# Performance work log

Measured on AMD Instinct MI355X. Metric: run time of the kernel, lower is better.

The kernel has to match this reference:

```python
import jax, jax.numpy as jnp
import numpy as np


def setup_inputs() -> dict:
    key = jax.random.key(0)
    inputs = jax.random.normal(key, (4096, 8192), dtype=jnp.float32)
    return {"inputs": inputs, "k": 512}


def reference(inputs, k):
    # Original: kth_smallest = sort_ascending(inputs)[..., n-1-k]
    # i.e. the (k+1)-th largest value per row. Equivalent via top_k.
    # Keep only elements STRICTLY greater than that threshold.
    thresh = jax.lax.top_k(inputs, k + 1)[0][..., -1]  # [batch]
    mask = (inputs > thresh[:, None]).astype(inputs.dtype)
    return inputs * mask
```

## Files before the change

### kernel.cpp

```cpp
#include <hip/hip_runtime.h>
#include <stdint.h>


constexpr int COLS  = 8192;
constexpr int TPB   = 256;
constexpr int EPT   = COLS / TPB;
constexpr int VPT   = EPT / 4;
constexpr int NBIN0 = 2048;
constexpr int CAP   = 2048;

__device__ __forceinline__ uint32_t map_f32(uint32_t u) {
  return (u & 0x80000000u) ? ~u : (u | 0x80000000u);
}
__device__ __forceinline__ float unmap_f32(uint32_t m) {
  return __uint_as_float((m & 0x80000000u) ? (m ^ 0x80000000u) : ~m);
}

__global__ __launch_bounds__(TPB)
void ksparse_kernel(const float* __restrict__ in, const int* __restrict__ kptr,
                    float* __restrict__ out) {
  __shared__ __align__(16) uint32_t hist[2 * NBIN0];
  __shared__ uint32_t th[3 * 128];
  __shared__ uint32_t wtot[4];
  __shared__ uint32_t s_packed;
  __shared__ uint32_t s_cnt;
  __shared__ uint32_t s_sel[3];

  const int t    = threadIdx.x;
  const int wave = t >> 6;
  const int lane = t & 63;
  const size_t rowbase = (size_t)blockIdx.x * COLS;

  const float4* inp = (const float4*)(in + rowbase);
  float4 v[VPT];
#pragma unroll
  for (int i = 0; i < VPT; ++i) v[i] = inp[t + i * TPB];

  uint4* h4 = (uint4*)hist;
#pragma unroll
  for (int i = 0; i < 4; ++i) h4[t + i * TPB] = make_uint4(0u, 0u, 0u, 0u);
  th[t] = 0u;
  if (t < 128) th[256 + t] = 0u;
  if (t == 0) { s_packed = 0u; s_cnt = 0u; }
  uint32_t kk = (uint32_t)(*kptr) + 1u;
  __syncthreads();

  uint32_t m[EPT];
  uint32_t* h = &hist[(wave >> 1) * NBIN0];
#pragma unroll
  for (int i = 0; i < VPT; ++i) {
    m[4 * i + 0] = map_f32(__float_as_uint(v[i].x));
    m[4 * i + 1] = map_f32(__float_as_uint(v[i].y));
    m[4 * i + 2] = map_f32(__float_as_uint(v[i].z));
    m[4 * i + 3] = map_f32(__float_as_uint(v[i].w));
    atomicAdd(&h[m[4 * i + 0] >> 21], 1u);
    atomicAdd(&h[m[4 * i + 1] >> 21], 1u);
    atomicAdd(&h[m[4 * i + 2] >> 21], 1u);
    atomicAdd(&h[m[4 * i + 3] >> 21], 1u);
  }
  __syncthreads();

  {
    const uint4* hv = (const uint4*)hist;
    uint4 a0 = hv[2 * t], a1 = hv[2 * t + 1];
    uint4 b0 = hv[512 + 2 * t], b1 = hv[512 + 2 * t + 1];
    uint32_t c0 = a0.x + b0.x, c1 = a0.y + b0.y, c2 = a0.z + b0.z, c3 = a0.w + b0.w;
    uint32_t c4 = a1.x + b1.x, c5 = a1.y + b1.y, c6 = a1.z + b1.z, c7 = a1.w + b1.w;
    uint32_t sl[8];
    sl[7] = c7;         sl[6] = sl[7] + c6; sl[5] = sl[6] + c5; sl[4] = sl[5] + c4;
    sl[3] = sl[4] + c3; sl[2] = sl[3] + c2; sl[1] = sl[2] + c1; sl[0] = sl[1] + c0;
    const uint32_t total = sl[0];

    uint32_t s = total;
#pragma unroll
    for (int off = 1; off < 64; off <<= 1) {
      uint32_t tmp = __shfl_down(s, off, 64);
      s += (lane + off < 64) ? tmp : 0u;
    }
    if (lane == 0) wtot[wave] = s;
    __syncthreads();

    uint32_t hi = 0;
#pragma unroll
    for (int w = 1; w < 4; ++w)
      if (w > wave) hi += wtot[w];
    const uint32_t excl = hi + (s - total);

    int best = -1;
#pragma unroll
    for (int j = 7; j >= 0; --j)
      if (best < 0 && excl + sl[j] >= kk) best = j;
    if (best >= 0) {
      const uint32_t above = excl + ((best < 7) ? sl[best + 1] : 0u);
      atomicMax(&s_packed, ((uint32_t)(t * 8 + best) << 14) | above);
    }
  }
  __syncthreads();

  const uint32_t pk = s_packed;
  const uint32_t d0 = pk >> 14;
  kk -= (pk & 0x3FFFu);

  uint32_t* cand = &hist[NBIN0];
#pragma unroll
  for (int i = 0; i < EPT; ++i) {
    if ((m[i] >> 21) == d0) {
      uint32_t idx = atomicAdd(&s_cnt, 1u);
      if (idx < CAP) cand[idx] = m[i] & 0x1FFFFFu;
    }
  }
  __syncthreads();
  const uint32_t Cc = (s_cnt < (uint32_t)CAP) ? s_cnt : (uint32_t)CAP;

  uint32_t tpref = 0;
#pragma unroll 1
  for (int j = 0; j < 3; ++j) {
    const int dsh = 14 - 7 * j;
    uint32_t* thj = &th[j * 128];
    for (uint32_t idx = t; idx < Cc; idx += TPB) {
      const uint32_t c = cand[idx];
      const bool ok = (j == 0) || ((c >> (dsh + 7)) == tpref);
      if (ok) atomicAdd(&thj[(c >> dsh) & 127u], 1u);
    }
    __syncthreads();

    if (wave == 0) {
      uint32_t a = thj[lane], b = thj[64 + lane];
      uint32_t sb = b, sa = a;
#pragma unroll
      for (int off = 1; off < 64; off <<= 1) {
        uint32_t t1 = __shfl_down(sb, off, 64);
        uint32_t t2 = __shfl_down(sa, off, 64);
        const bool inr = (lane + off < 64);
        sb += inr ? t1 : 0u;
        sa += inr ? t2 : 0u;
      }
      const uint32_t tb = __shfl(sb, 0, 64);
      sa += tb;
      const unsigned long long mb = __ballot(sb >= kk);
      uint32_t d, ab;
      if (mb) {
        const int hb = 63 - __builtin_clzll(mb);
        const uint32_t nx = __shfl(sb, (hb + 1) & 63, 64);
        d = 64 + hb;
        ab = (hb == 63) ? 0u : nx;
      } else {
        const unsigned long long ma = __ballot(sa >= kk);
        const int ha = 63 - __builtin_clzll(ma);
        const uint32_t nx = __shfl(sa, (ha + 1) & 63, 64);
        d = (uint32_t)ha;
        ab = (ha == 63) ? tb : nx;
      }
      if (lane == 0) s_sel[j] = (d << 16) | ab;
    }
    __syncthreads();

    const uint32_t sel = s_sel[j];
    tpref = (tpref << 7) | (sel >> 16);
    kk -= (sel & 0xFFFFu);
  }

  const uint32_t T = (d0 << 21) | tpref;

  float4* op = (float4*)(out + rowbase);
#pragma unroll
  for (int i = 0; i < VPT; ++i) {
    float4 w;
    uint32_t mm;
    mm = m[4 * i + 0]; w.x = (mm > T) ? unmap_f32(mm) : 0.0f;
    mm = m[4 * i + 1]; w.y = (mm > T) ? unmap_f32(mm) : 0.0f;
    mm = m[4 * i + 2]; w.z = (mm > T) ? unmap_f32(mm) : 0.0f;
    mm = m[4 * i + 3]; w.w = (mm > T) ? unmap_f32(mm) : 0.0f;
    op[t + i * TPB] = w;
  }
}

extern "C" void kernel_launch(void* const* d_in, const int* in_sizes, int n_in,
                              void* d_out, int out_size, void* d_ws, size_t ws_size,
                              hipStream_t stream) {
  const float* in  = (const float*)d_in[0];
  const int*   k   = (const int*)d_in[1];
  float*       out = (float*)d_out;
  int rows = in_sizes[0] / COLS;
  if (rows < 1) rows = 1;
  ksparse_kernel<<<rows, TPB, 0, stream>>>(in, k, out);
}
```

Measured before the change: 234.8 us.

## Process four rows per block with register double-buffered prefetch of next row

Each block now handles four rows. The next row's loads are issued into a second register buffer while the current row's selection passes run, so global memory latency overlaps with the histogram work. Output writes become nontemporal stores, and launch bounds request 4 waves per SIMD. The costs are doubled register pressure for the prefetch buffer (64 extra VGPRs) and a grid cut from 4096 to 1024 blocks, which could reduce latency hiding across blocks.

```diff
diff --git a/kernel.cpp b/kernel.cpp
--- a/kernel.cpp
+++ b/kernel.cpp
@@ -9,6 +9,8 @@
 constexpr int NBIN0 = 2048;
 constexpr int CAP   = 2048;
 
+typedef float f32x4 __attribute__((ext_vector_type(4)));
+
 __device__ __forceinline__ uint32_t map_f32(uint32_t u) {
   return (u & 0x80000000u) ? ~u : (u | 0x80000000u);
 }
@@ -16,7 +18,8 @@
   return __uint_as_float((m & 0x80000000u) ? (m ^ 0x80000000u) : ~m);
 }
 
-__global__ __launch_bounds__(TPB)
+template <int RPB>
+__global__ __launch_bounds__(TPB, 4)
 void ksparse_kernel(const float* __restrict__ in, const int* __restrict__ kptr,
                     float* __restrict__ out) {
   __shared__ __align__(16) uint32_t hist[2 * NBIN0];
@@ -29,149 +32,163 @@
   const int t    = threadIdx.x;
   const int wave = t >> 6;
   const int lane = t & 63;
-  const size_t rowbase = (size_t)blockIdx.x * COLS;
-
-  const float4* inp = (const float4*)(in + rowbase);
-  float4 v[VPT];
-#pragma unroll
-  for (int i = 0; i < VPT; ++i) v[i] = inp[t + i * TPB];
-
-  uint4* h4 = (uint4*)hist;
-#pragma unroll
-  for (int i = 0; i < 4; ++i) h4[t + i * TPB] = make_uint4(0u, 0u, 0u, 0u);
-  th[t] = 0u;
-  if (t < 128) th[256 + t] = 0u;
-  if (t == 0) { s_packed = 0u; s_cnt = 0u; }
-  uint32_t kk = (uint32_t)(*kptr) + 1u;
-  __syncthreads();
-
+  const size_t row0 = (size_t)blockIdx.x * RPB;
+
+  const uint32_t kbase = (uint32_t)(*kptr) + 1u;
+
+  float4   v[2][VPT];
   uint32_t m[EPT];
-  uint32_t* h = &hist[(wave >> 1) * NBIN0];
-#pragma unroll
-  for (int i = 0; i < VPT; ++i) {
-    m[4 * i + 0] = map_f32(__float_as_uint(v[i].x));
-    m[4 * i + 1] = map_f32(__float_as_uint(v[i].y));
-    m[4 * i + 2] = map_f32(__float_as_uint(v[i].z));
-    m[4 * i + 3] = map_f32(__float_as_uint(v[i].w));
-    atomicAdd(&h[m[4 * i + 0] >> 21], 1u);
-    atomicAdd(&h[m[4 * i + 1] >> 21], 1u);
-    atomicAdd(&h[m[4 * i + 2] >> 21], 1u);
-    atomicAdd(&h[m[4 * i + 3] >> 21], 1u);
+
+  {
+    const float4* inp = (const float4*)(in + row0 * COLS);
+#pragma unroll
+    for (int i = 0; i < VPT; ++i) v[0][i] = inp[t + i * TPB];
   }
-  __syncthreads();
-
-  {
-    const uint4* hv = (const uint4*)hist;
-    uint4 a0 = hv[2 * t], a1 = hv[2 * t + 1];
-    uint4 b0 = hv[512 + 2 * t], b1 = hv[512 + 2 * t + 1];
-    uint32_t c0 = a0.x + b0.x, c1 = a0.y + b0.y, c2 = a0.z + b0.z, c3 = a0.w + b0.w;
-    uint32_t c4 = a1.x + b1.x, c5 = a1.y + b1.y, c6 = a1.z + b1.z, c7 = a1.w + b1.w;
-    uint32_t sl[8];
-    sl[7] = c7;         sl[6] = sl[7] + c6; sl[5] = sl[6] + c5; sl[4] = sl[5] + c4;
-    sl[3] = sl[4] + c3; sl[2] = sl[3] + c2; sl[1] = sl[2] + c1; sl[0] = sl[1] + c0;
-    const uint32_t total = sl[0];
-
-    uint32_t s = total;
-#pragma unroll
-    for (int off = 1; off < 64; off <<= 1) {
-      uint32_t tmp = __shfl_down(s, off, 64);
-      s += (lane + off < 64) ? tmp : 0u;
-    }
-    if (lane == 0) wtot[wave] = s;
-    __syncthreads();
-
-    uint32_t hi = 0;
-#pragma unroll
-    for (int w = 1; w < 4; ++w)
-      if (w > wave) hi += wtot[w];
-    const uint32_t excl = hi + (s - total);
-
-    int best = -1;
-#pragma unroll
-    for (int j = 7; j >= 0; --j)
-      if (best < 0 && excl + sl[j] >= kk) best = j;
-    if (best >= 0) {
-      const uint32_t above = excl + ((best < 7) ? sl[best + 1] : 0u);
-      atomicMax(&s_packed, ((uint32_t)(t * 8 + best) << 14) | above);
-    }
-  }
-  __syncthreads();
-
-  const uint32_t pk = s_packed;
-  const uint32_t d0 = pk >> 14;
-  kk -= (pk & 0x3FFFu);
-
-  uint32_t* cand = &hist[NBIN0];
-#pragma unroll
-  for (int i = 0; i < EPT; ++i) {
-    if ((m[i] >> 21) == d0) {
-      uint32_t idx = atomicAdd(&s_cnt, 1u);
-      if (idx < CAP) cand[idx] = m[i] & 0x1FFFFFu;
-    }
-  }
-  __syncthreads();
-  const uint32_t Cc = (s_cnt < (uint32_t)CAP) ? s_cnt : (uint32_t)CAP;
-
-  uint32_t tpref = 0;
+
+#pragma unroll
+  for (int r = 0; r < RPB; ++r) {
+    uint4* h4 = (uint4*)hist;
+#pragma unroll
+    for (int i = 0; i < 4; ++i) h4[t + i * TPB] = make_uint4(0u, 0u, 0u, 0u);
+    th[t] = 0u;
+    if (t < 128) th[256 + t] = 0u;
+    if (t == 0) { s_packed = 0u; s_cnt = 0u; }
+    uint32_t kk = kbase;
+    __syncthreads();
+
+    uint32_t* h = &hist[(wave >> 1) * NBIN0];
+#pragma unroll
+    for (int i = 0; i < VPT; ++i) {
+      m[4 * i + 0] = map_f32(__float_as_uint(v[r & 1][i].x));
+      m[4 * i + 1] = map_f32(__float_as_uint(v[r & 1][i].y));
+      m[4 * i + 2] = map_f32(__float_as_uint(v[r & 1][i].z));
+      m[4 * i + 3] = map_f32(__float_as_uint(v[r & 1][i].w));
+      atomicAdd(&h[m[4 * i + 0] >> 21], 1u);
+      atomicAdd(&h[m[4 * i + 1] >> 21], 1u);
+      atomicAdd(&h[m[4 * i + 2] >> 21], 1u);
+      atomicAdd(&h[m[4 * i + 3] >> 21], 1u);
+    }
+
+    if (r + 1 < RPB) {
+      const float4* inp = (const float4*)(in + (row0 + (size_t)(r + 1)) * COLS);
+#pragma unroll
+      for (int i = 0; i < VPT; ++i) v[(r + 1) & 1][i] = inp[t + i * TPB];
+    }
+    __syncthreads();
+
+    {
+      const uint4* hv = (const uint4*)hist;
+      uint4 a0 = hv[2 * t], a1 = hv[2 * t + 1];
+      uint4 b0 = hv[512 + 2 * t], b1 = hv[512 + 2 * t + 1];
+      uint32_t c0 = a0.x + b0.x, c1 = a0.y + b0.y, c2 = a0.z + b0.z, c3 = a0.w + b0.w;
+      uint32_t c4 = a1.x + b1.x, c5 = a1.y + b1.y, c6 = a1.z + b1.z, c7 = a1.w + b1.w;
+      uint32_t sl[8];
+      sl[7] = c7;         sl[6] = sl[7] + c6; sl[5] = sl[6] + c5; sl[4] = sl[5] + c4;
+      sl[3] = sl[4] + c3; sl[2] = sl[3] + c2; sl[1] = sl[2] + c1; sl[0] = sl[1] + c0;
+      const uint32_t total = sl[0];
+
+      uint32_t s = total;
+#pragma unroll
+      for (int off = 1; off < 64; off <<= 1) {
+        uint32_t tmp = __shfl_down(s, off, 64);
+        s += (lane + off < 64) ? tmp : 0u;
+      }
+      if (lane == 0) wtot[wave] = s;
+      __syncthreads();
+
+      uint32_t hi = 0;
+#pragma unroll
+      for (int w = 1; w < 4; ++w)
+        if (w > wave) hi += wtot[w];
+      const uint32_t excl = hi + (s - total);
+
+      int best = -1;
+#pragma unroll
+      for (int j = 7; j >= 0; --j)
+        if (best < 0 && excl + sl[j] >= kk) best = j;
+      if (best >= 0) {
+        const uint32_t above = excl + ((best < 7) ? sl[best + 1] : 0u);
+        atomicMax(&s_packed, ((uint32_t)(t * 8 + best) << 14) | above);
+      }
+    }
+    __syncthreads();
+
+    const uint32_t pk = s_packed;
+    const uint32_t d0 = pk >> 14;
+    kk -= (pk & 0x3FFFu);
+
+    uint32_t* cand = &hist[NBIN0];
+#pragma unroll
+    for (int i = 0; i < EPT; ++i) {
+      if ((m[i] >> 21) == d0) {
+        uint32_t idx = atomicAdd(&s_cnt, 1u);
+        if (idx < CAP) cand[idx] = m[i] & 0x1FFFFFu;
+      }
+    }
+    __syncthreads();
+    const uint32_t Cc = (s_cnt < (uint32_t)CAP) ? s_cnt : (uint32_t)CAP;
+
+    uint32_t tpref = 0;
 #pragma unroll 1
-  for (int j = 0; j < 3; ++j) {
-    const int dsh = 14 - 7 * j;
-    uint32_t* thj = &th[j * 128];
-    for (uint32_t idx = t; idx < Cc; idx += TPB) {
-      const uint32_t c = cand[idx];
-      const bool ok = (j == 0) || ((c >> (dsh + 7)) == tpref);
-      if (ok) atomicAdd(&thj[(c >> dsh) & 127u], 1u);
-    }
-    __syncthreads();
-
-    if (wave == 0) {
-      uint32_t a = thj[lane], b = thj[64 + lane];
-      uint32_t sb = b, sa = a;
-#pragma unroll
-      for (int off = 1; off < 64; off <<= 1) {
-        uint32_t t1 = __shfl_down(sb, off, 64);
-        uint32_t t2 = __shfl_down(sa, off, 64);
-        const bool inr = (lane + off < 64);
-        sb += inr ? t1 : 0u;
-        sa += inr ? t2 : 0u;
-      }
-      const uint32_t tb = __shfl(sb, 0, 64);
-      sa += tb;
-      const unsigned long long mb = __ballot(sb >= kk);
-      uint32_t d, ab;
-      if (mb) {
-        const int hb = 63 - __builtin_clzll(mb);
-        const uint32_t nx = __shfl(sb, (hb + 1) & 63, 64);
-        d = 64 + hb;
-        ab = (hb == 63) ? 0u : nx;
-      } else {
-        const unsigned long long ma = __ballot(sa >= kk);
-        const int ha = 63 - __builtin_clzll(ma);
-        const uint32_t nx = __shfl(sa, (ha + 1) & 63, 64);
-        d = (uint32_t)ha;
-        ab = (ha == 63) ? tb : nx;
-      }
-      if (lane == 0) s_sel[j] = (d << 16) | ab;
-    }
-    __syncthreads();
-
-    const uint32_t sel = s_sel[j];
-    tpref = (tpref << 7) | (sel >> 16);
-    kk -= (sel & 0xFFFFu);
-  }
-
-  const uint32_t T = (d0 << 21) | tpref;
-
-  float4* op = (float4*)(out + rowbase);
-#pragma unroll
-  for (int i = 0; i < VPT; ++i) {
-    float4 w;
-    uint32_t mm;
-    mm = m[4 * i + 0]; w.x = (mm > T) ? unmap_f32(mm) : 0.0f;
-    mm = m[4 * i + 1]; w.y = (mm > T) ? unmap_f32(mm) : 0.0f;
-    mm = m[4 * i + 2]; w.z = (mm > T) ? unmap_f32(mm) : 0.0f;
-    mm = m[4 * i + 3]; w.w = (mm > T) ? unmap_f32(mm) : 0.0f;
-    op[t + i * TPB] = w;
+    for (int j = 0; j < 3; ++j) {
+      const int dsh = 14 - 7 * j;
+      uint32_t* thj = &th[j * 128];
+      for (uint32_t idx = t; idx < Cc; idx += TPB) {
+        const uint32_t c = cand[idx];
+        const bool ok = (j == 0) || ((c >> (dsh + 7)) == tpref);
+        if (ok) atomicAdd(&thj[(c >> dsh) & 127u], 1u);
+      }
+      __syncthreads();
+
+      if (wave == 0) {
+        uint32_t a = thj[lane], b = thj[64 + lane];
+        uint32_t sb = b, sa = a;
+#pragma unroll
+        for (int off = 1; off < 64; off <<= 1) {
+          uint32_t t1 = __shfl_down(sb, off, 64);
+          uint32_t t2 = __shfl_down(sa, off, 64);
+          const bool inr = (lane + off < 64);
+          sb += inr ? t1 : 0u;
+          sa += inr ? t2 : 0u;
+        }
+        const uint32_t tb = __shfl(sb, 0, 64);
+        sa += tb;
+        const unsigned long long mb = __ballot(sb >= kk);
+        uint32_t d, ab;
+        if (mb) {
+          const int hb = 63 - __builtin_clzll(mb);
+          const uint32_t nx = __shfl(sb, (hb + 1) & 63, 64);
+          d = 64 + hb;
+          ab = (hb == 63) ? 0u : nx;
+        } else {
+          const unsigned long long ma = __ballot(sa >= kk);
+          const int ha = 63 - __builtin_clzll(ma);
+          const uint32_t nx = __shfl(sa, (ha + 1) & 63, 64);
+          d = (uint32_t)ha;
+          ab = (ha == 63) ? tb : nx;
+        }
+        if (lane == 0) s_sel[j] = (d << 16) | ab;
+      }
+      __syncthreads();
+
+      const uint32_t sel = s_sel[j];
+      tpref = (tpref << 7) | (sel >> 16);
+      kk -= (sel & 0xFFFFu);
+    }
+
+    const uint32_t T = (d0 << 21) | tpref;
+
+    f32x4* op = (f32x4*)(out + (row0 + (size_t)r) * COLS);
+#pragma unroll
+    for (int i = 0; i < VPT; ++i) {
+      f32x4 w;
+      uint32_t mm;
+      mm = m[4 * i + 0]; w.x = (mm > T) ? unmap_f32(mm) : 0.0f;
+      mm = m[4 * i + 1]; w.y = (mm > T) ? unmap_f32(mm) : 0.0f;
+      mm = m[4 * i + 2]; w.z = (mm > T) ? unmap_f32(mm) : 0.0f;
+      mm = m[4 * i + 3]; w.w = (mm > T) ? unmap_f32(mm) : 0.0f;
+      __builtin_nontemporal_store(w, &op[t + i * TPB]);
+    }
   }
 }
 
@@ -183,5 +200,9 @@
   float*       out = (float*)d_out;
   int rows = in_sizes[0] / COLS;
   if (rows < 1) rows = 1;
-  ksparse_kernel<<<rows, TPB, 0, stream>>>(in, k, out);
-}
+  if ((rows & 3) == 0) {
+    ksparse_kernel<4><<<rows / 4, TPB, 0, stream>>>(in, k, out);
+  } else {
+    ksparse_kernel<1><<<rows, TPB, 0, stream>>>(in, k, out);
+  }
+}
```

New measurement: 258.7 us. 1.1x slower.

## Double block size, drop mapped-key registers, swizzle histogram, single-wave refinement

Applied to the files above, without the earlier changes.

Raises threads per block to 512 so each thread holds half as many elements. The per-element mapped-key array is dropped and bins are recomputed from the raw float bits, which lowers register pressure and should raise occupancy. The coarse histogram gets an XOR swizzle to spread LDS bank conflicts, and the coarse scan and the three fine radix passes now run inside a single wave, removing several block-wide barriers. The final mask compares floats against the unmapped threshold. The cost is that the fine refinement is serialized on one wave and the bin mapping is recomputed during candidate collection.

```diff
diff --git a/kernel.cpp b/kernel.cpp
--- a/kernel.cpp
+++ b/kernel.cpp
@@ -3,7 +3,7 @@
 
 
 constexpr int COLS  = 8192;
-constexpr int TPB   = 256;
+constexpr int TPB   = 512;
 constexpr int EPT   = COLS / TPB;
 constexpr int VPT   = EPT / 4;
 constexpr int NBIN0 = 2048;
@@ -15,134 +15,148 @@
 __device__ __forceinline__ float unmap_f32(uint32_t m) {
   return __uint_as_float((m & 0x80000000u) ? (m ^ 0x80000000u) : ~m);
 }
+__device__ __forceinline__ uint32_t bin11(uint32_t u) {
+  const uint32_t s = u >> 21;
+  return (u & 0x80000000u) ? (0x7FFu ^ s) : (s | 0x400u);
+}
+__device__ __forceinline__ uint32_t hswz(uint32_t w) {
+  return w ^ ((w >> 3) & 0x1Cu);
+}
 
-__global__ __launch_bounds__(TPB)
+__global__ __launch_bounds__(TPB, 8)
 void ksparse_kernel(const float* __restrict__ in, const int* __restrict__ kptr,
                     float* __restrict__ out) {
   __shared__ __align__(16) uint32_t hist[2 * NBIN0];
   __shared__ uint32_t th[3 * 128];
-  __shared__ uint32_t wtot[4];
   __shared__ uint32_t s_packed;
   __shared__ uint32_t s_cnt;
-  __shared__ uint32_t s_sel[3];
+  __shared__ uint32_t s_T;
 
   const int t    = threadIdx.x;
   const int wave = t >> 6;
   const int lane = t & 63;
   const size_t rowbase = (size_t)blockIdx.x * COLS;
 
+  uint4* h4 = (uint4*)hist;
+  h4[t] = make_uint4(0u, 0u, 0u, 0u);
+  h4[t + TPB] = make_uint4(0u, 0u, 0u, 0u);
+  if (t < 384) th[t] = 0u;
+  if (t == 0) { s_packed = 0u; s_cnt = 0u; }
+  const uint32_t kbase = (uint32_t)(*kptr) + 1u;
+  __syncthreads();
+
   const float4* inp = (const float4*)(in + rowbase);
   float4 v[VPT];
 #pragma unroll
   for (int i = 0; i < VPT; ++i) v[i] = inp[t + i * TPB];
 
-  uint4* h4 = (uint4*)hist;
-#pragma unroll
-  for (int i = 0; i < 4; ++i) h4[t + i * TPB] = make_uint4(0u, 0u, 0u, 0u);
-  th[t] = 0u;
-  if (t < 128) th[256 + t] = 0u;
-  if (t == 0) { s_packed = 0u; s_cnt = 0u; }
-  uint32_t kk = (uint32_t)(*kptr) + 1u;
-  __syncthreads();
-
-  uint32_t m[EPT];
-  uint32_t* h = &hist[(wave >> 1) * NBIN0];
+  uint32_t* h = &hist[(wave >> 2) * NBIN0];
 #pragma unroll
   for (int i = 0; i < VPT; ++i) {
-    m[4 * i + 0] = map_f32(__float_as_uint(v[i].x));
-    m[4 * i + 1] = map_f32(__float_as_uint(v[i].y));
-    m[4 * i + 2] = map_f32(__float_as_uint(v[i].z));
-    m[4 * i + 3] = map_f32(__float_as_uint(v[i].w));
-    atomicAdd(&h[m[4 * i + 0] >> 21], 1u);
-    atomicAdd(&h[m[4 * i + 1] >> 21], 1u);
-    atomicAdd(&h[m[4 * i + 2] >> 21], 1u);
-    atomicAdd(&h[m[4 * i + 3] >> 21], 1u);
+    atomicAdd(&h[hswz(bin11(__float_as_uint(v[i].x)))], 1u);
+    atomicAdd(&h[hswz(bin11(__float_as_uint(v[i].y)))], 1u);
+    atomicAdd(&h[hswz(bin11(__float_as_uint(v[i].z)))], 1u);
+    atomicAdd(&h[hswz(bin11(__float_as_uint(v[i].w)))], 1u);
   }
   __syncthreads();
 
-  {
-    const uint4* hv = (const uint4*)hist;
-    uint4 a0 = hv[2 * t], a1 = hv[2 * t + 1];
-    uint4 b0 = hv[512 + 2 * t], b1 = hv[512 + 2 * t + 1];
-    uint32_t c0 = a0.x + b0.x, c1 = a0.y + b0.y, c2 = a0.z + b0.z, c3 = a0.w + b0.w;
-    uint32_t c4 = a1.x + b1.x, c5 = a1.y + b1.y, c6 = a1.z + b1.z, c7 = a1.w + b1.w;
-    uint32_t sl[8];
-    sl[7] = c7;         sl[6] = sl[7] + c6; sl[5] = sl[6] + c5; sl[4] = sl[5] + c4;
-    sl[3] = sl[4] + c3; sl[2] = sl[3] + c2; sl[1] = sl[2] + c1; sl[0] = sl[1] + c0;
-    const uint32_t total = sl[0];
-
+  if (wave == 0) {
+    const uint4* r0 = (const uint4*)&hist[0];
+    const uint4* r1 = (const uint4*)&hist[NBIN0];
+    uint32_t qs[8];
+    uint32_t total = 0;
+#pragma unroll
+    for (int q = 0; q < 8; ++q) {
+      const uint32_t Q = (uint32_t)(8 * lane + q);
+      const uint32_t Qs = Q ^ (uint32_t)(lane & 7);
+      const uint4 a = r0[Qs];
+      const uint4 b = r1[Qs];
+      qs[q] = (a.x + b.x) + (a.y + b.y) + (a.z + b.z) + (a.w + b.w);
+      total += qs[q];
+    }
     uint32_t s = total;
 #pragma unroll
     for (int off = 1; off < 64; off <<= 1) {
-      uint32_t tmp = __shfl_down(s, off, 64);
+      const uint32_t tmp = __shfl_down(s, off, 64);
       s += (lane + off < 64) ? tmp : 0u;
     }
-    if (lane == 0) wtot[wave] = s;
-    __syncthreads();
-
-    uint32_t hi = 0;
+    const unsigned long long mb = __ballot(s >= kbase);
+    const int lstar = 63 - __builtin_clzll(mb);
+    if (lane == lstar) {
+      uint32_t run = s - total;
+      int qq = -1; uint32_t qab = 0;
 #pragma unroll
-    for (int w = 1; w < 4; ++w)
-      if (w > wave) hi += wtot[w];
-    const uint32_t excl = hi + (s - total);
-
-    int best = -1;
-#pragma unroll
-    for (int j = 7; j >= 0; --j)
-      if (best < 0 && excl + sl[j] >= kk) best = j;
-    if (best >= 0) {
-      const uint32_t above = excl + ((best < 7) ? sl[best + 1] : 0u);
-      atomicMax(&s_packed, ((uint32_t)(t * 8 + best) << 14) | above);
+      for (int q = 7; q >= 0; --q) {
+        const uint32_t nrun = run + qs[q];
+        if (qq < 0 && nrun >= kbase) { qq = q; qab = run; }
+        run = nrun;
+      }
+      const uint32_t Qs = (uint32_t)(8 * lane + qq) ^ (uint32_t)(lane & 7);
+      const uint4 a = r0[Qs];
+      const uint4 b = r1[Qs];
+      const uint32_t c0 = a.x + b.x, c1 = a.y + b.y, c2 = a.z + b.z, c3 = a.w + b.w;
+      const uint32_t s3 = qab + c3;
+      const uint32_t s2 = s3 + c2, s1 = s2 + c1;
+      uint32_t e, above;
+      if (s3 >= kbase)      { e = 3u; above = qab; }
+      else if (s2 >= kbase) { e = 2u; above = s3; }
+      else if (s1 >= kbase) { e = 1u; above = s2; }
+      else                  { e = 0u; above = s1; }
+      const uint32_t d0 = (uint32_t)(lane * 32 + qq * 4) + e;
+      s_packed = (d0 << 14) | above;
     }
   }
   __syncthreads();
 
   const uint32_t pk = s_packed;
   const uint32_t d0 = pk >> 14;
-  kk -= (pk & 0x3FFFu);
 
   uint32_t* cand = &hist[NBIN0];
 #pragma unroll
-  for (int i = 0; i < EPT; ++i) {
-    if ((m[i] >> 21) == d0) {
-      uint32_t idx = atomicAdd(&s_cnt, 1u);
-      if (idx < CAP) cand[idx] = m[i] & 0x1FFFFFu;
-    }
+  for (int i = 0; i < VPT; ++i) {
+    uint32_t u;
+    u = __float_as_uint(v[i].x);
+    if (bin11(u) == d0) { const uint32_t x = atomicAdd(&s_cnt, 1u); if (x < CAP) cand[x] = map_f32(u) & 0x1FFFFFu; }
+    u = __float_as_uint(v[i].y);
+    if (bin11(u) == d0) { const uint32_t x = atomicAdd(&s_cnt, 1u); if (x < CAP) cand[x] = map_f32(u) & 0x1FFFFFu; }
+    u = __float_as_uint(v[i].z);
+    if (bin11(u) == d0) { const uint32_t x = atomicAdd(&s_cnt, 1u); if (x < CAP) cand[x] = map_f32(u) & 0x1FFFFFu; }
+    u = __float_as_uint(v[i].w);
+    if (bin11(u) == d0) { const uint32_t x = atomicAdd(&s_cnt, 1u); if (x < CAP) cand[x] = map_f32(u) & 0x1FFFFFu; }
   }
   __syncthreads();
-  const uint32_t Cc = (s_cnt < (uint32_t)CAP) ? s_cnt : (uint32_t)CAP;
 
-  uint32_t tpref = 0;
+  if (wave == 0) {
+    const uint32_t Cc = (s_cnt < (uint32_t)CAP) ? s_cnt : (uint32_t)CAP;
+    uint32_t kk = kbase - (pk & 0x3FFFu);
+    uint32_t tpref = 0;
 #pragma unroll 1
-  for (int j = 0; j < 3; ++j) {
-    const int dsh = 14 - 7 * j;
-    uint32_t* thj = &th[j * 128];
-    for (uint32_t idx = t; idx < Cc; idx += TPB) {
-      const uint32_t c = cand[idx];
-      const bool ok = (j == 0) || ((c >> (dsh + 7)) == tpref);
-      if (ok) atomicAdd(&thj[(c >> dsh) & 127u], 1u);
-    }
-    __syncthreads();
-
-    if (wave == 0) {
-      uint32_t a = thj[lane], b = thj[64 + lane];
+    for (int j = 0; j < 3; ++j) {
+      const int dsh = 14 - 7 * j;
+      uint32_t* thj = &th[j * 128];
+      for (uint32_t idx = (uint32_t)lane; idx < Cc; idx += 64u) {
+        const uint32_t c = cand[idx];
+        const bool ok = (j == 0) || ((c >> (dsh + 7)) == tpref);
+        if (ok) atomicAdd(&thj[(c >> dsh) & 127u], 1u);
+      }
+      const uint32_t a = thj[lane], b = thj[64 + lane];
       uint32_t sb = b, sa = a;
 #pragma unroll
       for (int off = 1; off < 64; off <<= 1) {
-        uint32_t t1 = __shfl_down(sb, off, 64);
-        uint32_t t2 = __shfl_down(sa, off, 64);
+        const uint32_t t1 = __shfl_down(sb, off, 64);
+        const uint32_t t2 = __shfl_down(sa, off, 64);
         const bool inr = (lane + off < 64);
         sb += inr ? t1 : 0u;
         sa += inr ? t2 : 0u;
       }
       const uint32_t tb = __shfl(sb, 0, 64);
       sa += tb;
-      const unsigned long long mb = __ballot(sb >= kk);
+      const unsigned long long mbj = __ballot(sb >= kk);
       uint32_t d, ab;
-      if (mb) {
-        const int hb = 63 - __builtin_clzll(mb);
+      if (mbj) {
+        const int hb = 63 - __builtin_clzll(mbj);
         const uint32_t nx = __shfl(sb, (hb + 1) & 63, 64);
-        d = 64 + hb;
+        d = 64u + (uint32_t)hb;
         ab = (hb == 63) ? 0u : nx;
       } else {
         const unsigned long long ma = __ballot(sa >= kk);
@@ -151,26 +165,22 @@
         d = (uint32_t)ha;
         ab = (ha == 63) ? tb : nx;
       }
-      if (lane == 0) s_sel[j] = (d << 16) | ab;
+      tpref = (tpref << 7) | d;
+      kk -= ab;
     }
-    __syncthreads();
+    if (lane == 0) s_T = (d0 << 21) | tpref;
+  }
+  __syncthreads();
 
-    const uint32_t sel = s_sel[j];
-    tpref = (tpref << 7) | (sel >> 16);
-    kk -= (sel & 0xFFFFu);
-  }
-
-  const uint32_t T = (d0 << 21) | tpref;
-
+  const float thr = unmap_f32(s_T);
   float4* op = (float4*)(out + rowbase);
 #pragma unroll
   for (int i = 0; i < VPT; ++i) {
     float4 w;
-    uint32_t mm;
-    mm = m[4 * i + 0]; w.x = (mm > T) ? unmap_f32(mm) : 0.0f;
-    mm = m[4 * i + 1]; w.y = (mm > T) ? unmap_f32(mm) : 0.0f;
-    mm = m[4 * i + 2]; w.z = (mm > T) ? unmap_f32(mm) : 0.0f;
-    mm = m[4 * i + 3]; w.w = (mm > T) ? unmap_f32(mm) : 0.0f;
+    w.x = (v[i].x > thr) ? v[i].x : 0.0f;
+    w.y = (v[i].y > thr) ? v[i].y : 0.0f;
+    w.z = (v[i].z > thr) ? v[i].z : 0.0f;
+    w.w = (v[i].w > thr) ? v[i].w : 0.0f;
     op[t + i * TPB] = w;
   }
 }
```

New measurement: 257.8 us. +9.8%, slower.
